# Kernel optimization log

Measured on AMD Instinct MI355X. Metric: run time of the kernel, lower is better.

Reference implementation:

```python
import jax, jax.numpy as jnp
import numpy as np

H = 32  # hidden_size
NUM_LAYERS = 3
INPUT_SIZE = 64
STD = 0.1


def setup_inputs() -> dict:
    key = jax.random.key(0)
    ks = jax.random.split(key, 2 * NUM_LAYERS + 2)
    inp = {}
    inp["x"] = jax.random.normal(ks[0], (256, 2048, INPUT_SIZE), dtype=jnp.float32)
    in_dim = INPUT_SIZE
    for l in range(NUM_LAYERS):
        inp[f"W_ih{l}"] = STD * jax.random.normal(ks[1 + 2 * l], (4 * H, in_dim), dtype=jnp.float32)
        inp[f"W_hh{l}"] = STD * jax.random.normal(ks[2 + 2 * l], (4 * H, H), dtype=jnp.float32)
        inp[f"b{l}"] = jnp.zeros((4 * H,), dtype=jnp.float32)  # b_ih + b_hh, both init to 0
        in_dim = H
    inp["W_out"] = STD * jax.random.normal(ks[-1], (1, H), dtype=jnp.float32)
    inp["b_out"] = jnp.zeros((1,), dtype=jnp.float32)
    return inp


def _lstm_layer(x, W_ih, W_hh, b):
    # x: [B, T, D_in] -> h_seq: [B, T, H]
    B = x.shape[0]
    # precompute input-to-gate projections for all timesteps (one big GEMM)
    xg = jnp.einsum('btd,gd->btg', x, W_ih) + b          # [B, T, 4H]
    xg = jnp.swapaxes(xg, 0, 1)                           # [T, B, 4H]
    W_hh_T = W_hh.T                                       # [H, 4H]

    def step(carry, xg_t):
        h, c = carry
        g = xg_t + h @ W_hh_T                             # [B, 4H]
        i = jax.nn.sigmoid(g[:, 0 * H:1 * H])
        f = jax.nn.sigmoid(g[:, 1 * H:2 * H])
        gg = jnp.tanh(g[:, 2 * H:3 * H])
        o = jax.nn.sigmoid(g[:, 3 * H:4 * H])
        c = f * c + i * gg
        h = o * jnp.tanh(c)
        return (h, c), h

    h0 = jnp.zeros((B, H), dtype=x.dtype)
    c0 = jnp.zeros((B, H), dtype=x.dtype)
    _, h_seq = jax.lax.scan(step, (h0, c0), xg)           # h_seq: [T, B, H]
    return jnp.swapaxes(h_seq, 0, 1)                      # [B, T, H]


def reference(x, W_ih0, W_hh0, b0, W_ih1, W_hh1, b1, W_ih2, W_hh2, b2, W_out, b_out):
    h = _lstm_layer(x, W_ih0, W_hh0, b0)
    h = _lstm_layer(h, W_ih1, W_hh1, b1)
    h = _lstm_layer(h, W_ih2, W_hh2, b2)
    last = h[:, -1, :]                                    # [B, H]
    return last @ W_out.T + b_out                         # [B, 1]
```

## Files before the change

kernel.cpp:

```cpp
#include <hip/hip_runtime.h>


typedef float v2f __attribute__((ext_vector_type(2)));

constexpr int T_SEQ  = 2048;
constexpr int HID    = 32;
constexpr int CH     = 16;
constexpr int NCHUNK = T_SEQ / CH;
constexpr int NPHASE = NCHUNK + 5;

__device__ __forceinline__ float sigmoid_f(float x) { return 1.0f / (1.0f + __expf(-x)); }
__device__ __forceinline__ float tanh_f(float x)    { return 1.0f - 2.0f / (__expf(2.0f * x) + 1.0f); }

#define GLOAD_LDS16(gsrc, ldst)                                                              \
    __builtin_amdgcn_global_load_lds((const __attribute__((address_space(1))) void*)(gsrc), \
                                     (__attribute__((address_space(3))) void*)(ldst),        \
                                     16, 0, 0)
#define KEEPV(x) asm volatile("" : "+v"(x))

template<int N4>
__device__ __forceinline__ void feed_chunk(int l, const float* in, int stride,
                                           v2f (*xg)[64],
                                           const v2f (&wA)[N4 * 2], const v2f (&wB)[N4 * 2],
                                           float bAv, float bBv)
{
#pragma unroll
    for (int tt = 0; tt < CH; ++tt) {
        const float4* xt = reinterpret_cast<const float4*>(in + tt * stride);
        v2f aA = {bAv, 0.f}, aB = {bBv, 0.f};
#pragma unroll
        for (int i = 0; i < N4; ++i) {
            const float4 v = xt[i];
            const v2f lo = {v.x, v.y}, hi = {v.z, v.w};
            aA = lo * wA[2*i] + aA;  aA = hi * wA[2*i+1] + aA;
            aB = lo * wB[2*i] + aB;  aB = hi * wB[2*i+1] + aB;
        }
        v2f o; o.x = aA.x + aA.y; o.y = aB.x + aB.y;
        xg[tt][l] = o;
    }
}

__device__ __forceinline__ void recur_chunk(int l, const v2f (*xg)[64],
                                            float* hbp, float (*hr)[HID],
                                            const v2f (&wA)[16], const v2f (&wB)[16],
                                            float& c, float& hreg)
{
#pragma unroll
    for (int tt = 0; tt < CH; ++tt) {
        const v2f xgv = xg[tt][l];
        asm volatile("s_waitcnt lgkmcnt(0)" ::: "memory");
        const float4* h4 = reinterpret_cast<const float4*>(hbp);
        v2f aA = {xgv.x, 0.f}, aB = {xgv.y, 0.f};
#pragma unroll
        for (int i = 0; i < 8; ++i) {
            const float4 v = h4[i];
            const v2f lo = {v.x, v.y}, hi = {v.z, v.w};
            aA = lo * wA[2*i] + aA;  aA = hi * wA[2*i+1] + aA;
            aB = lo * wB[2*i] + aB;  aB = hi * wB[2*i+1] + aB;
        }
        const float ga = aA.x + aA.y, gb = aB.x + aB.y;
        const float sA = sigmoid_f(ga);
        const float tb = tanh_f(l < 32 ? gb : 0.5f * gb);
        const float vB = (l < 32) ? tb : fmaf(0.5f, tb, 0.5f);
        const float fv = __shfl_xor(sA, 32);
        const float ov = __shfl_xor(vB, 32);
        const float cn = fmaf(fv, c, sA * vB);
        const float hn = ov * tanh_f(cn);
        if (l < HID) {
            c = cn; hreg = hn;
            hbp[l] = hn;
            if (hr) hr[tt][l] = hn;
        }
    }
}

__global__ __launch_bounds__(384, 2)
void lstm3_spec_kernel(const float* __restrict__ x,
                       const float* __restrict__ W_ih0, const float* __restrict__ W_hh0, const float* __restrict__ b0,
                       const float* __restrict__ W_ih1, const float* __restrict__ W_hh1, const float* __restrict__ b1,
                       const float* __restrict__ W_ih2, const float* __restrict__ W_hh2, const float* __restrict__ b2,
                       const float* __restrict__ W_out, const float* __restrict__ b_out,
                       float* __restrict__ out)
{
    const int bi = blockIdx.x;
    const int w  = threadIdx.x >> 6;
    const int l  = threadIdx.x & 63;

    __shared__ float xstage[CH * 64];
    __shared__ v2f   xg0[2][CH][64];
    __shared__ v2f   xg1[2][CH][64];
    __shared__ v2f   xg2[2][CH][64];
    __shared__ float h0r[2][CH][HID];
    __shared__ float h1r[2][CH][HID];
    __shared__ float hb[3][HID];

    if (w == 0) {
        __builtin_amdgcn_s_setprio(1);
        v2f wA[16], wB[16];
        const v2f* pA = reinterpret_cast<const v2f*>(W_hh0 + l * 32);
        const v2f* pB = reinterpret_cast<const v2f*>(W_hh0 + (l + 64) * 32);
#pragma unroll
        for (int i = 0; i < 16; ++i) { wA[i] = pA[i]; KEEPV(wA[i]); wB[i] = pB[i]; KEEPV(wB[i]); }
        if (l < HID) hb[0][l] = 0.f;
        float c = 0.f, hreg = 0.f;
        __syncthreads();
        for (int p = 0; p < NPHASE; ++p) {
            const int ci = p - 1;
            if (ci >= 0 && ci < NCHUNK)
                recur_chunk(l, xg0[ci & 1], hb[0], h0r[ci & 1], wA, wB, c, hreg);
            __syncthreads();
        }
    } else if (w == 1) {
        __builtin_amdgcn_s_setprio(1);
        v2f wA[16], wB[16];
        const v2f* pA = reinterpret_cast<const v2f*>(W_hh1 + l * 32);
        const v2f* pB = reinterpret_cast<const v2f*>(W_hh1 + (l + 64) * 32);
#pragma unroll
        for (int i = 0; i < 16; ++i) { wA[i] = pA[i]; KEEPV(wA[i]); wB[i] = pB[i]; KEEPV(wB[i]); }
        if (l < HID) hb[1][l] = 0.f;
        float c = 0.f, hreg = 0.f;
        __syncthreads();
        for (int p = 0; p < NPHASE; ++p) {
            const int ci = p - 3;
            if (ci >= 0 && ci < NCHUNK)
                recur_chunk(l, xg1[ci & 1], hb[1], h1r[ci & 1], wA, wB, c, hreg);
            __syncthreads();
        }
    } else if (w == 2) {
        __builtin_amdgcn_s_setprio(1);
        v2f wA[16], wB[16];
        const v2f* pA = reinterpret_cast<const v2f*>(W_hh2 + l * 32);
        const v2f* pB = reinterpret_cast<const v2f*>(W_hh2 + (l + 64) * 32);
#pragma unroll
        for (int i = 0; i < 16; ++i) { wA[i] = pA[i]; KEEPV(wA[i]); wB[i] = pB[i]; KEEPV(wB[i]); }
        const float woutv = (l < HID) ? W_out[l] : 0.f;
        if (l < HID) hb[2][l] = 0.f;
        float c = 0.f, hreg = 0.f;
        __syncthreads();
        for (int p = 0; p < NPHASE; ++p) {
            const int ci = p - 5;
            if (ci >= 0 && ci < NCHUNK)
                recur_chunk(l, xg2[ci & 1], hb[2], (float(*)[HID])nullptr, wA, wB, c, hreg);
            __syncthreads();
        }
        float s = (l < HID) ? hreg * woutv : 0.f;
#pragma unroll
        for (int off = 16; off; off >>= 1) s += __shfl_xor(s, off);
        if (l == 0) out[bi] = s + b_out[0];
    } else if (w == 3) {
        v2f wA[32], wB[32];
        const v2f* pA = reinterpret_cast<const v2f*>(W_ih0 + l * 64);
        const v2f* pB = reinterpret_cast<const v2f*>(W_ih0 + (l + 64) * 64);
#pragma unroll
        for (int i = 0; i < 32; ++i) { wA[i] = pA[i]; KEEPV(wA[i]); wB[i] = pB[i]; KEEPV(wB[i]); }
        const float bAv = b0[l], bBv = b0[l + 64];
        const float* src = x + (size_t)bi * T_SEQ * 64;
        __syncthreads();
        for (int p = 0; p < NPHASE; ++p) {
            if (p < NCHUNK) {
                const float* ns = src + (size_t)p * CH * 64;
#pragma unroll
                for (int i = 0; i < 4; ++i)
                    GLOAD_LDS16(ns + i * 256 + l * 4, &xstage[i * 256 + l * 4]);
                asm volatile("s_waitcnt vmcnt(0)" ::: "memory");
                feed_chunk<16>(l, xstage, 64, xg0[p & 1], wA, wB, bAv, bBv);
            }
            __syncthreads();
        }
    } else if (w == 4) {
        v2f wA[16], wB[16];
        const v2f* pA = reinterpret_cast<const v2f*>(W_ih1 + l * 32);
        const v2f* pB = reinterpret_cast<const v2f*>(W_ih1 + (l + 64) * 32);
#pragma unroll
        for (int i = 0; i < 16; ++i) { wA[i] = pA[i]; KEEPV(wA[i]); wB[i] = pB[i]; KEEPV(wB[i]); }
        const float bAv = b1[l], bBv = b1[l + 64];
        __syncthreads();
        for (int p = 0; p < NPHASE; ++p) {
            const int ci = p - 2;
            if (ci >= 0 && ci < NCHUNK)
                feed_chunk<8>(l, &h0r[ci & 1][0][0], HID, xg1[ci & 1], wA, wB, bAv, bBv);
            __syncthreads();
        }
    } else {
        v2f wA[16], wB[16];
        const v2f* pA = reinterpret_cast<const v2f*>(W_ih2 + l * 32);
        const v2f* pB = reinterpret_cast<const v2f*>(W_ih2 + (l + 64) * 32);
#pragma unroll
        for (int i = 0; i < 16; ++i) { wA[i] = pA[i]; KEEPV(wA[i]); wB[i] = pB[i]; KEEPV(wB[i]); }
        const float bAv = b2[l], bBv = b2[l + 64];
        __syncthreads();
        for (int p = 0; p < NPHASE; ++p) {
            const int ci = p - 4;
            if (ci >= 0 && ci < NCHUNK)
                feed_chunk<8>(l, &h1r[ci & 1][0][0], HID, xg2[ci & 1], wA, wB, bAv, bBv);
            __syncthreads();
        }
    }
}

extern "C" void kernel_launch(void* const* d_in, const int* in_sizes, int n_in,
                              void* d_out, int out_size, void* d_ws, size_t ws_size,
                              hipStream_t stream) {
    const float* x      = (const float*)d_in[0];
    const float* W_ih0  = (const float*)d_in[1];
    const float* W_hh0  = (const float*)d_in[2];
    const float* b0     = (const float*)d_in[3];
    const float* W_ih1  = (const float*)d_in[4];
    const float* W_hh1  = (const float*)d_in[5];
    const float* b1     = (const float*)d_in[6];
    const float* W_ih2  = (const float*)d_in[7];
    const float* W_hh2  = (const float*)d_in[8];
    const float* b2     = (const float*)d_in[9];
    const float* W_out  = (const float*)d_in[10];
    const float* b_out  = (const float*)d_in[11];

    lstm3_spec_kernel<<<256, 384, 0, stream>>>(x,
                                               W_ih0, W_hh0, b0,
                                               W_ih1, W_hh1, b1,
                                               W_ih2, W_hh2, b2,
                                               W_out, b_out,
                                               (float*)d_out);
}
```

Baseline: 699.8 us.

## Fuse next-layer input projection into recurrence waves and broadcast h via bpermute

Cuts the block from six waves to four. Each recurrent wave now computes the next layer's input projection right after its own step, which removes the separate feed waves and the h0r/h1r LDS round trip and shortens the pipeline by two phases. The hidden state is now broadcast to registers with ds_bpermute instead of being written to and read back from LDS. The layer-0 x loads are double-buffered so the global load overlaps the feed computation. The gate dot products are also split into two accumulators for more ILP. In exchange, each recurrent step carries more work on the serial critical path and uses more registers.

Result: slower. 1.022 ms (+46.0%).

```diff
diff --git a/kernel.cpp b/kernel.cpp
--- a/kernel.cpp
+++ b/kernel.cpp
@@ -7,7 +7,7 @@
 constexpr int HID    = 32;
 constexpr int CH     = 16;
 constexpr int NCHUNK = T_SEQ / CH;
-constexpr int NPHASE = NCHUNK + 5;
+constexpr int NPHASE = NCHUNK + 3;
 
 __device__ __forceinline__ float sigmoid_f(float x) { return 1.0f / (1.0f + __expf(-x)); }
 __device__ __forceinline__ float tanh_f(float x)    { return 1.0f - 2.0f / (__expf(2.0f * x) + 1.0f); }
@@ -18,47 +18,29 @@
                                      16, 0, 0)
 #define KEEPV(x) asm volatile("" : "+v"(x))
 
-template<int N4>
-__device__ __forceinline__ void feed_chunk(int l, const float* in, int stride,
-                                           v2f (*xg)[64],
-                                           const v2f (&wA)[N4 * 2], const v2f (&wB)[N4 * 2],
-                                           float bAv, float bBv)
+template<bool PROD>
+__device__ __forceinline__ void rec_chunk(int l, int a0v,
+    const v2f* __restrict__ xg_in, v2f* __restrict__ xg_out,
+    const v2f (&whA)[16], const v2f (&whB)[16],
+    const v2f* wiA, const v2f* wiB, float biA, float biB,
+    v2f (&hb2)[16], float& c, float& hreg)
 {
+    v2f xgr[CH];
+#pragma unroll
+    for (int tt = 0; tt < CH; ++tt) xgr[tt] = xg_in[tt * 64 + l];
+
 #pragma unroll
     for (int tt = 0; tt < CH; ++tt) {
-        const float4* xt = reinterpret_cast<const float4*>(in + tt * stride);
-        v2f aA = {bAv, 0.f}, aB = {bBv, 0.f};
-#pragma unroll
-        for (int i = 0; i < N4; ++i) {
-            const float4 v = xt[i];
-            const v2f lo = {v.x, v.y}, hi = {v.z, v.w};
-            aA = lo * wA[2*i] + aA;  aA = hi * wA[2*i+1] + aA;
-            aB = lo * wB[2*i] + aB;  aB = hi * wB[2*i+1] + aB;
-        }
-        v2f o; o.x = aA.x + aA.y; o.y = aB.x + aB.y;
-        xg[tt][l] = o;
-    }
-}
-
-__device__ __forceinline__ void recur_chunk(int l, const v2f (*xg)[64],
-                                            float* hbp, float (*hr)[HID],
-                                            const v2f (&wA)[16], const v2f (&wB)[16],
-                                            float& c, float& hreg)
-{
-#pragma unroll
-    for (int tt = 0; tt < CH; ++tt) {
-        const v2f xgv = xg[tt][l];
-        asm volatile("s_waitcnt lgkmcnt(0)" ::: "memory");
-        const float4* h4 = reinterpret_cast<const float4*>(hbp);
-        v2f aA = {xgv.x, 0.f}, aB = {xgv.y, 0.f};
-#pragma unroll
-        for (int i = 0; i < 8; ++i) {
-            const float4 v = h4[i];
-            const v2f lo = {v.x, v.y}, hi = {v.z, v.w};
-            aA = lo * wA[2*i] + aA;  aA = hi * wA[2*i+1] + aA;
-            aB = lo * wB[2*i] + aB;  aB = hi * wB[2*i+1] + aB;
-        }
-        const float ga = aA.x + aA.y, gb = aB.x + aB.y;
+        v2f aA0 = {xgr[tt].x, 0.f}, aA1 = {0.f, 0.f};
+        v2f aB0 = {xgr[tt].y, 0.f}, aB1 = {0.f, 0.f};
+#pragma unroll
+        for (int j = 0; j < 16; j += 2) {
+            aA0 = hb2[j]   * whA[j]   + aA0;  aB0 = hb2[j]   * whB[j]   + aB0;
+            aA1 = hb2[j+1] * whA[j+1] + aA1;  aB1 = hb2[j+1] * whB[j+1] + aB1;
+        }
+        const float ga = (aA0.x + aA1.x) + (aA0.y + aA1.y);
+        const float gb = (aB0.x + aB1.x) + (aB0.y + aB1.y);
+
         const float sA = sigmoid_f(ga);
         const float tb = tanh_f(l < 32 ? gb : 0.5f * gb);
         const float vB = (l < 32) ? tb : fmaf(0.5f, tb, 0.5f);
@@ -66,88 +48,138 @@
         const float ov = __shfl_xor(vB, 32);
         const float cn = fmaf(fv, c, sA * vB);
         const float hn = ov * tanh_f(cn);
-        if (l < HID) {
-            c = cn; hreg = hn;
-            hbp[l] = hn;
-            if (hr) hr[tt][l] = hn;
+        c = cn; hreg = hn;
+
+        const int hbits = __float_as_int(hn);
+#pragma unroll
+        for (int j = 0; j < 16; ++j) {
+            const float bx = __int_as_float(__builtin_amdgcn_ds_bpermute(a0v + 8*j,     hbits));
+            const float by = __int_as_float(__builtin_amdgcn_ds_bpermute(a0v + 8*j + 4, hbits));
+            hb2[j] = (v2f){bx, by};
+        }
+
+        if constexpr (PROD) {
+            v2f pA = {biA, 0.f}, pB = {biB, 0.f};
+#pragma unroll
+            for (int j = 0; j < 16; ++j) { pA = hb2[j] * wiA[j] + pA; pB = hb2[j] * wiB[j] + pB; }
+            xg_out[tt * 64 + l] = (v2f){pA.x + pA.y, pB.x + pB.y};
         }
     }
 }
 
-__global__ __launch_bounds__(384, 2)
-void lstm3_spec_kernel(const float* __restrict__ x,
-                       const float* __restrict__ W_ih0, const float* __restrict__ W_hh0, const float* __restrict__ b0,
-                       const float* __restrict__ W_ih1, const float* __restrict__ W_hh1, const float* __restrict__ b1,
-                       const float* __restrict__ W_ih2, const float* __restrict__ W_hh2, const float* __restrict__ b2,
-                       const float* __restrict__ W_out, const float* __restrict__ b_out,
-                       float* __restrict__ out)
+__device__ __forceinline__ void feed0_chunk(int l, const float* __restrict__ xs,
+    v2f* __restrict__ xg_out,
+    const v2f (&wA)[32], const v2f (&wB)[32], float bAv, float bBv)
+{
+#pragma unroll
+    for (int tt = 0; tt < CH; ++tt) {
+        const float4* xt = reinterpret_cast<const float4*>(xs + tt * 64);
+        v2f aA0 = {bAv, 0.f}, aA1 = {0.f, 0.f}, aB0 = {bBv, 0.f}, aB1 = {0.f, 0.f};
+#pragma unroll
+        for (int i = 0; i < 16; ++i) {
+            const float4 v = xt[i];
+            const v2f lo = {v.x, v.y}, hi = {v.z, v.w};
+            aA0 = lo * wA[2*i] + aA0;  aA1 = hi * wA[2*i+1] + aA1;
+            aB0 = lo * wB[2*i] + aB0;  aB1 = hi * wB[2*i+1] + aB1;
+        }
+        xg_out[tt * 64 + l] = (v2f){(aA0.x + aA1.x) + (aA0.y + aA1.y),
+                                    (aB0.x + aB1.x) + (aB0.y + aB1.y)};
+    }
+}
+
+__global__ __launch_bounds__(256, 1)
+void lstm3_fused_kernel(const float* __restrict__ x,
+    const float* __restrict__ W_ih0, const float* __restrict__ W_hh0, const float* __restrict__ b0,
+    const float* __restrict__ W_ih1, const float* __restrict__ W_hh1, const float* __restrict__ b1,
+    const float* __restrict__ W_ih2, const float* __restrict__ W_hh2, const float* __restrict__ b2,
+    const float* __restrict__ W_out, const float* __restrict__ b_out,
+    float* __restrict__ out)
 {
     const int bi = blockIdx.x;
     const int w  = threadIdx.x >> 6;
     const int l  = threadIdx.x & 63;
 
-    __shared__ float xstage[CH * 64];
     __shared__ v2f   xg0[2][CH][64];
     __shared__ v2f   xg1[2][CH][64];
     __shared__ v2f   xg2[2][CH][64];
-    __shared__ float h0r[2][CH][HID];
-    __shared__ float h1r[2][CH][HID];
-    __shared__ float hb[3][HID];
+    __shared__ float xstage[2][CH * 64];
+
+    int a0v = 0; asm volatile("" : "+v"(a0v));
 
     if (w == 0) {
-        __builtin_amdgcn_s_setprio(1);
-        v2f wA[16], wB[16];
-        const v2f* pA = reinterpret_cast<const v2f*>(W_hh0 + l * 32);
-        const v2f* pB = reinterpret_cast<const v2f*>(W_hh0 + (l + 64) * 32);
-#pragma unroll
-        for (int i = 0; i < 16; ++i) { wA[i] = pA[i]; KEEPV(wA[i]); wB[i] = pB[i]; KEEPV(wB[i]); }
-        if (l < HID) hb[0][l] = 0.f;
+        v2f whA[16], whB[16], wiA[16], wiB[16];
+        const v2f* hA = reinterpret_cast<const v2f*>(W_hh0 + l * 32);
+        const v2f* hB = reinterpret_cast<const v2f*>(W_hh0 + (l + 64) * 32);
+        const v2f* iA = reinterpret_cast<const v2f*>(W_ih1 + l * 32);
+        const v2f* iB = reinterpret_cast<const v2f*>(W_ih1 + (l + 64) * 32);
+#pragma unroll
+        for (int i = 0; i < 16; ++i) {
+            whA[i] = hA[i]; KEEPV(whA[i]); whB[i] = hB[i]; KEEPV(whB[i]);
+            wiA[i] = iA[i]; KEEPV(wiA[i]); wiB[i] = iB[i]; KEEPV(wiB[i]);
+        }
+        const float biA = b1[l], biB = b1[l + 64];
+        v2f hb2[16];
+#pragma unroll
+        for (int i = 0; i < 16; ++i) hb2[i] = (v2f){0.f, 0.f};
         float c = 0.f, hreg = 0.f;
         __syncthreads();
         for (int p = 0; p < NPHASE; ++p) {
             const int ci = p - 1;
             if (ci >= 0 && ci < NCHUNK)
-                recur_chunk(l, xg0[ci & 1], hb[0], h0r[ci & 1], wA, wB, c, hreg);
+                rec_chunk<true>(l, a0v, &xg0[ci & 1][0][0], &xg1[ci & 1][0][0],
+                                whA, whB, wiA, wiB, biA, biB, hb2, c, hreg);
             __syncthreads();
         }
     } else if (w == 1) {
-        __builtin_amdgcn_s_setprio(1);
-        v2f wA[16], wB[16];
-        const v2f* pA = reinterpret_cast<const v2f*>(W_hh1 + l * 32);
-        const v2f* pB = reinterpret_cast<const v2f*>(W_hh1 + (l + 64) * 32);
-#pragma unroll
-        for (int i = 0; i < 16; ++i) { wA[i] = pA[i]; KEEPV(wA[i]); wB[i] = pB[i]; KEEPV(wB[i]); }
-        if (l < HID) hb[1][l] = 0.f;
+        v2f whA[16], whB[16], wiA[16], wiB[16];
+        const v2f* hA = reinterpret_cast<const v2f*>(W_hh1 + l * 32);
+        const v2f* hB = reinterpret_cast<const v2f*>(W_hh1 + (l + 64) * 32);
+        const v2f* iA = reinterpret_cast<const v2f*>(W_ih2 + l * 32);
+        const v2f* iB = reinterpret_cast<const v2f*>(W_ih2 + (l + 64) * 32);
+#pragma unroll
+        for (int i = 0; i < 16; ++i) {
+            whA[i] = hA[i]; KEEPV(whA[i]); whB[i] = hB[i]; KEEPV(whB[i]);
+            wiA[i] = iA[i]; KEEPV(wiA[i]); wiB[i] = iB[i]; KEEPV(wiB[i]);
+        }
+        const float biA = b2[l], biB = b2[l + 64];
+        v2f hb2[16];
+#pragma unroll
+        for (int i = 0; i < 16; ++i) hb2[i] = (v2f){0.f, 0.f};
+        float c = 0.f, hreg = 0.f;
+        __syncthreads();
+        for (int p = 0; p < NPHASE; ++p) {
+            const int ci = p - 2;
+            if (ci >= 0 && ci < NCHUNK)
+                rec_chunk<true>(l, a0v, &xg1[ci & 1][0][0], &xg2[ci & 1][0][0],
+                                whA, whB, wiA, wiB, biA, biB, hb2, c, hreg);
+            __syncthreads();
+        }
+    } else if (w == 2) {
+        v2f whA[16], whB[16];
+        const v2f* hA = reinterpret_cast<const v2f*>(W_hh2 + l * 32);
+        const v2f* hB = reinterpret_cast<const v2f*>(W_hh2 + (l + 64) * 32);
+#pragma unroll
+        for (int i = 0; i < 16; ++i) {
+            whA[i] = hA[i]; KEEPV(whA[i]); whB[i] = hB[i]; KEEPV(whB[i]);
+        }
+        const float woutv = W_out[l & 31];
+        v2f hb2[16];
+#pragma unroll
+        for (int i = 0; i < 16; ++i) hb2[i] = (v2f){0.f, 0.f};
         float c = 0.f, hreg = 0.f;
         __syncthreads();
         for (int p = 0; p < NPHASE; ++p) {
             const int ci = p - 3;
             if (ci >= 0 && ci < NCHUNK)
-                recur_chunk(l, xg1[ci & 1], hb[1], h1r[ci & 1], wA, wB, c, hreg);
-            __syncthreads();
-        }
-    } else if (w == 2) {
-        __builtin_amdgcn_s_setprio(1);
-        v2f wA[16], wB[16];
-        const v2f* pA = reinterpret_cast<const v2f*>(W_hh2 + l * 32);
-        const v2f* pB = reinterpret_cast<const v2f*>(W_hh2 + (l + 64) * 32);
-#pragma unroll
-        for (int i = 0; i < 16; ++i) { wA[i] = pA[i]; KEEPV(wA[i]); wB[i] = pB[i]; KEEPV(wB[i]); }
-        const float woutv = (l < HID) ? W_out[l] : 0.f;
-        if (l < HID) hb[2][l] = 0.f;
-        float c = 0.f, hreg = 0.f;
-        __syncthreads();
-        for (int p = 0; p < NPHASE; ++p) {
-            const int ci = p - 5;
-            if (ci >= 0 && ci < NCHUNK)
-                recur_chunk(l, xg2[ci & 1], hb[2], (float(*)[HID])nullptr, wA, wB, c, hreg);
+                rec_chunk<false>(l, a0v, &xg2[ci & 1][0][0], nullptr,
+                                 whA, whB, nullptr, nullptr, 0.f, 0.f, hb2, c, hreg);
             __syncthreads();
         }
         float s = (l < HID) ? hreg * woutv : 0.f;
 #pragma unroll
-        for (int off = 16; off; off >>= 1) s += __shfl_xor(s, off);
+        for (int off = 32; off; off >>= 1) s += __shfl_xor(s, off);
         if (l == 0) out[bi] = s + b_out[0];
-    } else if (w == 3) {
+    } else {
         v2f wA[32], wB[32];
         const v2f* pA = reinterpret_cast<const v2f*>(W_ih0 + l * 64);
         const v2f* pB = reinterpret_cast<const v2f*>(W_ih0 + (l + 64) * 64);
@@ -155,44 +187,20 @@
         for (int i = 0; i < 32; ++i) { wA[i] = pA[i]; KEEPV(wA[i]); wB[i] = pB[i]; KEEPV(wB[i]); }
         const float bAv = b0[l], bBv = b0[l + 64];
         const float* src = x + (size_t)bi * T_SEQ * 64;
-        __syncthreads();
-        for (int p = 0; p < NPHASE; ++p) {
-            if (p < NCHUNK) {
-                const float* ns = src + (size_t)p * CH * 64;
+#pragma unroll
+        for (int i = 0; i < 4; ++i)
+            GLOAD_LDS16(src + i * 256 + l * 4, &xstage[0][i * 256 + l * 4]);
+        __syncthreads();
+        for (int p = 0; p < NPHASE; ++p) {
+            if (p + 1 < NCHUNK) {
+                const float* ns = src + (size_t)(p + 1) * CH * 64;
+                float* dst = &xstage[(p + 1) & 1][0];
 #pragma unroll
                 for (int i = 0; i < 4; ++i)
-                    GLOAD_LDS16(ns + i * 256 + l * 4, &xstage[i * 256 + l * 4]);
-                asm volatile("s_waitcnt vmcnt(0)" ::: "memory");
-                feed_chunk<16>(l, xstage, 64, xg0[p & 1], wA, wB, bAv, bBv);
+                    GLOAD_LDS16(ns + i * 256 + l * 4, dst + i * 256 + l * 4);
             }
-            __syncthreads();
-        }
-    } else if (w == 4) {
-        v2f wA[16], wB[16];
-        const v2f* pA = reinterpret_cast<const v2f*>(W_ih1 + l * 32);
-        const v2f* pB = reinterpret_cast<const v2f*>(W_ih1 + (l + 64) * 32);
-#pragma unroll
-        for (int i = 0; i < 16; ++i) { wA[i] = pA[i]; KEEPV(wA[i]); wB[i] = pB[i]; KEEPV(wB[i]); }
-        const float bAv = b1[l], bBv = b1[l + 64];
-        __syncthreads();
-        for (int p = 0; p < NPHASE; ++p) {
-            const int ci = p - 2;
-            if (ci >= 0 && ci < NCHUNK)
-                feed_chunk<8>(l, &h0r[ci & 1][0][0], HID, xg1[ci & 1], wA, wB, bAv, bBv);
-            __syncthreads();
-        }
-    } else {
-        v2f wA[16], wB[16];
-        const v2f* pA = reinterpret_cast<const v2f*>(W_ih2 + l * 32);
-        const v2f* pB = reinterpret_cast<const v2f*>(W_ih2 + (l + 64) * 32);
-#pragma unroll
-        for (int i = 0; i < 16; ++i) { wA[i] = pA[i]; KEEPV(wA[i]); wB[i] = pB[i]; KEEPV(wB[i]); }
-        const float bAv = b2[l], bBv = b2[l + 64];
-        __syncthreads();
-        for (int p = 0; p < NPHASE; ++p) {
-            const int ci = p - 4;
-            if (ci >= 0 && ci < NCHUNK)
-                feed_chunk<8>(l, &h1r[ci & 1][0][0], HID, xg2[ci & 1], wA, wB, bAv, bBv);
+            if (p < NCHUNK)
+                feed0_chunk(l, xstage[p & 1], &xg0[p & 1][0][0], wA, wB, bAv, bBv);
             __syncthreads();
         }
     }
@@ -214,10 +222,10 @@
     const float* W_out  = (const float*)d_in[10];
     const float* b_out  = (const float*)d_in[11];
 
-    lstm3_spec_kernel<<<256, 384, 0, stream>>>(x,
-                                               W_ih0, W_hh0, b0,
-                                               W_ih1, W_hh1, b1,
-                                               W_ih2, W_hh2, b2,
-                                               W_out, b_out,
-                                               (float*)d_out);
-}
+    lstm3_fused_kernel<<<256, 256, 0, stream>>>(x,
+                                                W_ih0, W_hh0, b0,
+                                                W_ih1, W_hh1, b1,
+                                                W_ih2, W_hh2, b2,
+                                                W_out, b_out,
+                                                (float*)d_out);
+}
```

## Broadcast recurrent hidden state via readlane instead of LDS, prefetch x double-buffered

Applied to the files above, without the earlier changes.

The recurrent waves now broadcast the new hidden state to every lane with 32 readlane instructions into SGPR-backed registers. This replaces writing it to LDS and reading it back behind an lgkmcnt wait, taking the LDS round trip off the serial critical path of each timestep. Gate math uses hardware rcp and per-lane constants instead of selects. The input-projection wave double-buffers the x staging area so the next chunk's global load overlaps the current chunk's compute. The readlane chain adds scalar-path serialization and register pressure, and all lanes now compute c/h redundantly.

Result: slower. 757.6 us (+8.3%).

```diff
diff --git a/kernel.cpp b/kernel.cpp
--- a/kernel.cpp
+++ b/kernel.cpp
@@ -4,13 +4,9 @@
 typedef float v2f __attribute__((ext_vector_type(2)));
 
 constexpr int T_SEQ  = 2048;
-constexpr int HID    = 32;
 constexpr int CH     = 16;
 constexpr int NCHUNK = T_SEQ / CH;
 constexpr int NPHASE = NCHUNK + 5;
-
-__device__ __forceinline__ float sigmoid_f(float x) { return 1.0f / (1.0f + __expf(-x)); }
-__device__ __forceinline__ float tanh_f(float x)    { return 1.0f - 2.0f / (__expf(2.0f * x) + 1.0f); }
 
 #define GLOAD_LDS16(gsrc, ldst)                                                              \
     __builtin_amdgcn_global_load_lds((const __attribute__((address_space(1))) void*)(gsrc), \
@@ -18,132 +14,183 @@
                                      16, 0, 0)
 #define KEEPV(x) asm volatile("" : "+v"(x))
 
-template<int N4>
-__device__ __forceinline__ void feed_chunk(int l, const float* in, int stride,
-                                           v2f (*xg)[64],
-                                           const v2f (&wA)[N4 * 2], const v2f (&wB)[N4 * 2],
-                                           float bAv, float bBv)
-{
+__device__ __forceinline__ float rcp_f(float x) { return __builtin_amdgcn_rcpf(x); }
+
+template<bool RING>
+__device__ __forceinline__ void rec_chunk_rl(int l,
+    const v2f* __restrict__ xg_in,
+    float* __restrict__ ring_out,
+    const float (&whA)[32], const float (&whB)[32],
+    float (&hs)[32], float& c, float& hreg,
+    float mt, float ca, float cb)
+{
+    v2f xgr[CH];
+#pragma unroll
+    for (int tt = 0; tt < CH; ++tt) xgr[tt] = xg_in[tt * 64 + l];
+
 #pragma unroll
     for (int tt = 0; tt < CH; ++tt) {
-        const float4* xt = reinterpret_cast<const float4*>(in + tt * stride);
-        v2f aA = {bAv, 0.f}, aB = {bBv, 0.f};
-#pragma unroll
-        for (int i = 0; i < N4; ++i) {
-            const float4 v = xt[i];
-            const v2f lo = {v.x, v.y}, hi = {v.z, v.w};
-            aA = lo * wA[2*i] + aA;  aA = hi * wA[2*i+1] + aA;
-            aB = lo * wB[2*i] + aB;  aB = hi * wB[2*i+1] + aB;
-        }
-        v2f o; o.x = aA.x + aA.y; o.y = aB.x + aB.y;
-        xg[tt][l] = o;
-    }
-}
-
-__device__ __forceinline__ void recur_chunk(int l, const v2f (*xg)[64],
-                                            float* hbp, float (*hr)[HID],
-                                            const v2f (&wA)[16], const v2f (&wB)[16],
-                                            float& c, float& hreg)
+        float aA0 = xgr[tt].x, aA1 = 0.f, aB0 = xgr[tt].y, aB1 = 0.f;
+#pragma unroll
+        for (int k = 0; k < 32; k += 2) {
+            aA0 = fmaf(hs[k],     whA[k],     aA0);
+            aB0 = fmaf(hs[k],     whB[k],     aB0);
+            aA1 = fmaf(hs[k + 1], whA[k + 1], aA1);
+            aB1 = fmaf(hs[k + 1], whB[k + 1], aB1);
+        }
+        const float ga = aA0 + aA1, gb = aB0 + aB1;
+
+        const float sA = rcp_f(1.0f + __expf(-ga));
+        const float eb = __expf(mt * gb);
+        const float tb = fmaf(-2.0f, rcp_f(eb + 1.0f), 1.0f);
+        const float vB = fmaf(ca, tb, cb);
+
+        const float fv = __shfl_xor(sA, 32);
+        const float ov = __shfl_xor(vB, 32);
+        const float cn = fmaf(fv, c, sA * vB);
+        const float ec = __expf(2.0f * cn);
+        const float hn = ov * fmaf(-2.0f, rcp_f(ec + 1.0f), 1.0f);
+        c = cn; hreg = hn;
+
+        if constexpr (RING) { if (l < 32) ring_out[tt * 32 + l] = hn; }
+
+        const int hbits = __float_as_int(hn);
+#pragma unroll
+        for (int k = 0; k < 32; ++k)
+            hs[k] = __int_as_float(__builtin_amdgcn_readlane(hbits, k));
+    }
+}
+
+__device__ __forceinline__ void feed_h_chunk(int l, const float* __restrict__ hr,
+    v2f* __restrict__ xg_out, const v2f (&wA)[16], const v2f (&wB)[16],
+    float bA, float bB)
 {
 #pragma unroll
     for (int tt = 0; tt < CH; ++tt) {
-        const v2f xgv = xg[tt][l];
-        asm volatile("s_waitcnt lgkmcnt(0)" ::: "memory");
-        const float4* h4 = reinterpret_cast<const float4*>(hbp);
-        v2f aA = {xgv.x, 0.f}, aB = {xgv.y, 0.f};
+        const float4* h4 = reinterpret_cast<const float4*>(hr + tt * 32);
+        v2f a0 = {bA, 0.f}, a1 = {0.f, 0.f}, b0 = {bB, 0.f}, b1 = {0.f, 0.f};
 #pragma unroll
         for (int i = 0; i < 8; ++i) {
             const float4 v = h4[i];
             const v2f lo = {v.x, v.y}, hi = {v.z, v.w};
-            aA = lo * wA[2*i] + aA;  aA = hi * wA[2*i+1] + aA;
-            aB = lo * wB[2*i] + aB;  aB = hi * wB[2*i+1] + aB;
-        }
-        const float ga = aA.x + aA.y, gb = aB.x + aB.y;
-        const float sA = sigmoid_f(ga);
-        const float tb = tanh_f(l < 32 ? gb : 0.5f * gb);
-        const float vB = (l < 32) ? tb : fmaf(0.5f, tb, 0.5f);
-        const float fv = __shfl_xor(sA, 32);
-        const float ov = __shfl_xor(vB, 32);
-        const float cn = fmaf(fv, c, sA * vB);
-        const float hn = ov * tanh_f(cn);
-        if (l < HID) {
-            c = cn; hreg = hn;
-            hbp[l] = hn;
-            if (hr) hr[tt][l] = hn;
-        }
+            a0 = lo * wA[2*i] + a0;  a1 = hi * wA[2*i+1] + a1;
+            b0 = lo * wB[2*i] + b0;  b1 = hi * wB[2*i+1] + b1;
+        }
+        xg_out[tt * 64 + l] = (v2f){(a0.x + a1.x) + (a0.y + a1.y),
+                                    (b0.x + b1.x) + (b0.y + b1.y)};
+    }
+}
+
+__device__ __forceinline__ void feed0_chunk(int l, const float* __restrict__ xs,
+    v2f* __restrict__ xg_out, const v2f (&wA)[32], const v2f (&wB)[32],
+    float bA, float bB)
+{
+#pragma unroll
+    for (int tt = 0; tt < CH; ++tt) {
+        const float4* xt = reinterpret_cast<const float4*>(xs + tt * 64);
+        v2f a0 = {bA, 0.f}, a1 = {0.f, 0.f}, b0 = {bB, 0.f}, b1 = {0.f, 0.f};
+#pragma unroll
+        for (int i = 0; i < 16; ++i) {
+            const float4 v = xt[i];
+            const v2f lo = {v.x, v.y}, hi = {v.z, v.w};
+            a0 = lo * wA[2*i] + a0;  a1 = hi * wA[2*i+1] + a1;
+            b0 = lo * wB[2*i] + b0;  b1 = hi * wB[2*i+1] + b1;
+        }
+        xg_out[tt * 64 + l] = (v2f){(a0.x + a1.x) + (a0.y + a1.y),
+                                    (b0.x + b1.x) + (b0.y + b1.y)};
     }
 }
 
 __global__ __launch_bounds__(384, 2)
-void lstm3_spec_kernel(const float* __restrict__ x,
-                       const float* __restrict__ W_ih0, const float* __restrict__ W_hh0, const float* __restrict__ b0,
-                       const float* __restrict__ W_ih1, const float* __restrict__ W_hh1, const float* __restrict__ b1,
-                       const float* __restrict__ W_ih2, const float* __restrict__ W_hh2, const float* __restrict__ b2,
-                       const float* __restrict__ W_out, const float* __restrict__ b_out,
-                       float* __restrict__ out)
+void lstm3_rl_kernel(const float* __restrict__ x,
+    const float* __restrict__ W_ih0, const float* __restrict__ W_hh0, const float* __restrict__ b0,
+    const float* __restrict__ W_ih1, const float* __restrict__ W_hh1, const float* __restrict__ b1,
+    const float* __restrict__ W_ih2, const float* __restrict__ W_hh2, const float* __restrict__ b2,
+    const float* __restrict__ W_out, const float* __restrict__ b_out,
+    float* __restrict__ out)
 {
     const int bi = blockIdx.x;
     const int w  = threadIdx.x >> 6;
     const int l  = threadIdx.x & 63;
 
-    __shared__ float xstage[CH * 64];
     __shared__ v2f   xg0[2][CH][64];
     __shared__ v2f   xg1[2][CH][64];
     __shared__ v2f   xg2[2][CH][64];
-    __shared__ float h0r[2][CH][HID];
-    __shared__ float h1r[2][CH][HID];
-    __shared__ float hb[3][HID];
+    __shared__ float h0r[2][CH][32];
+    __shared__ float h1r[2][CH][32];
+    __shared__ float xstage[2][CH * 64];
 
     if (w == 0) {
         __builtin_amdgcn_s_setprio(1);
-        v2f wA[16], wB[16];
-        const v2f* pA = reinterpret_cast<const v2f*>(W_hh0 + l * 32);
-        const v2f* pB = reinterpret_cast<const v2f*>(W_hh0 + (l + 64) * 32);
-#pragma unroll
-        for (int i = 0; i < 16; ++i) { wA[i] = pA[i]; KEEPV(wA[i]); wB[i] = pB[i]; KEEPV(wB[i]); }
-        if (l < HID) hb[0][l] = 0.f;
+        float whA[32], whB[32];
+#pragma unroll
+        for (int k = 0; k < 32; ++k) {
+            whA[k] = W_hh0[l * 32 + k];        KEEPV(whA[k]);
+            whB[k] = W_hh0[(l + 64) * 32 + k]; KEEPV(whB[k]);
+        }
+        const float mt = (l < 32) ? 2.f : 1.f;
+        const float ca = (l < 32) ? 1.f : 0.5f;
+        const float cb = (l < 32) ? 0.f : 0.5f;
+        float hs[32];
+#pragma unroll
+        for (int k = 0; k < 32; ++k) hs[k] = 0.f;
         float c = 0.f, hreg = 0.f;
         __syncthreads();
         for (int p = 0; p < NPHASE; ++p) {
             const int ci = p - 1;
             if (ci >= 0 && ci < NCHUNK)
-                recur_chunk(l, xg0[ci & 1], hb[0], h0r[ci & 1], wA, wB, c, hreg);
+                rec_chunk_rl<true>(l, &xg0[ci & 1][0][0], &h0r[ci & 1][0][0],
+                                   whA, whB, hs, c, hreg, mt, ca, cb);
             __syncthreads();
         }
     } else if (w == 1) {
         __builtin_amdgcn_s_setprio(1);
-        v2f wA[16], wB[16];
-        const v2f* pA = reinterpret_cast<const v2f*>(W_hh1 + l * 32);
-        const v2f* pB = reinterpret_cast<const v2f*>(W_hh1 + (l + 64) * 32);
-#pragma unroll
-        for (int i = 0; i < 16; ++i) { wA[i] = pA[i]; KEEPV(wA[i]); wB[i] = pB[i]; KEEPV(wB[i]); }
-        if (l < HID) hb[1][l] = 0.f;
+        float whA[32], whB[32];
+#pragma unroll
+        for (int k = 0; k < 32; ++k) {
+            whA[k] = W_hh1[l * 32 + k];        KEEPV(whA[k]);
+            whB[k] = W_hh1[(l + 64) * 32 + k]; KEEPV(whB[k]);
+        }
+        const float mt = (l < 32) ? 2.f : 1.f;
+        const float ca = (l < 32) ? 1.f : 0.5f;
+        const float cb = (l < 32) ? 0.f : 0.5f;
+        float hs[32];
+#pragma unroll
+        for (int k = 0; k < 32; ++k) hs[k] = 0.f;
         float c = 0.f, hreg = 0.f;
         __syncthreads();
         for (int p = 0; p < NPHASE; ++p) {
             const int ci = p - 3;
             if (ci >= 0 && ci < NCHUNK)
-                recur_chunk(l, xg1[ci & 1], hb[1], h1r[ci & 1], wA, wB, c, hreg);
+                rec_chunk_rl<true>(l, &xg1[ci & 1][0][0], &h1r[ci & 1][0][0],
+                                   whA, whB, hs, c, hreg, mt, ca, cb);
             __syncthreads();
         }
     } else if (w == 2) {
         __builtin_amdgcn_s_setprio(1);
-        v2f wA[16], wB[16];
-        const v2f* pA = reinterpret_cast<const v2f*>(W_hh2 + l * 32);
-        const v2f* pB = reinterpret_cast<const v2f*>(W_hh2 + (l + 64) * 32);
-#pragma unroll
-        for (int i = 0; i < 16; ++i) { wA[i] = pA[i]; KEEPV(wA[i]); wB[i] = pB[i]; KEEPV(wB[i]); }
-        const float woutv = (l < HID) ? W_out[l] : 0.f;
-        if (l < HID) hb[2][l] = 0.f;
+        float whA[32], whB[32];
+#pragma unroll
+        for (int k = 0; k < 32; ++k) {
+            whA[k] = W_hh2[l * 32 + k];        KEEPV(whA[k]);
+            whB[k] = W_hh2[(l + 64) * 32 + k]; KEEPV(whB[k]);
+        }
+        const float mt = (l < 32) ? 2.f : 1.f;
+        const float ca = (l < 32) ? 1.f : 0.5f;
+        const float cb = (l < 32) ? 0.f : 0.5f;
+        const float woutv = W_out[l & 31];
+        float hs[32];
+#pragma unroll
+        for (int k = 0; k < 32; ++k) hs[k] = 0.f;
         float c = 0.f, hreg = 0.f;
         __syncthreads();
         for (int p = 0; p < NPHASE; ++p) {
             const int ci = p - 5;
             if (ci >= 0 && ci < NCHUNK)
-                recur_chunk(l, xg2[ci & 1], hb[2], (float(*)[HID])nullptr, wA, wB, c, hreg);
-            __syncthreads();
-        }
-        float s = (l < HID) ? hreg * woutv : 0.f;
+                rec_chunk_rl<false>(l, &xg2[ci & 1][0][0], nullptr,
+                                    whA, whB, hs, c, hreg, mt, ca, cb);
+            __syncthreads();
+        }
+        float s = (l < 32) ? hreg * woutv : 0.f;
 #pragma unroll
         for (int off = 16; off; off >>= 1) s += __shfl_xor(s, off);
         if (l == 0) out[bi] = s + b_out[0];
@@ -155,16 +202,20 @@
         for (int i = 0; i < 32; ++i) { wA[i] = pA[i]; KEEPV(wA[i]); wB[i] = pB[i]; KEEPV(wB[i]); }
         const float bAv = b0[l], bBv = b0[l + 64];
         const float* src = x + (size_t)bi * T_SEQ * 64;
-        __syncthreads();
-        for (int p = 0; p < NPHASE; ++p) {
-            if (p < NCHUNK) {
-                const float* ns = src + (size_t)p * CH * 64;
+#pragma unroll
+        for (int i = 0; i < 4; ++i)
+            GLOAD_LDS16(src + i * 256 + l * 4, &xstage[0][i * 256 + l * 4]);
+        __syncthreads();
+        for (int p = 0; p < NPHASE; ++p) {
+            if (p + 1 < NCHUNK) {
+                const float* ns = src + (size_t)(p + 1) * CH * 64;
+                float* dst = &xstage[(p + 1) & 1][0];
 #pragma unroll
                 for (int i = 0; i < 4; ++i)
-                    GLOAD_LDS16(ns + i * 256 + l * 4, &xstage[i * 256 + l * 4]);
-                asm volatile("s_waitcnt vmcnt(0)" ::: "memory");
-                feed_chunk<16>(l, xstage, 64, xg0[p & 1], wA, wB, bAv, bBv);
+                    GLOAD_LDS16(ns + i * 256 + l * 4, dst + i * 256 + l * 4);
             }
+            if (p < NCHUNK)
+                feed0_chunk(l, xstage[p & 1], &xg0[p & 1][0][0], wA, wB, bAv, bBv);
             __syncthreads();
         }
     } else if (w == 4) {
@@ -178,7 +229,7 @@
         for (int p = 0; p < NPHASE; ++p) {
             const int ci = p - 2;
             if (ci >= 0 && ci < NCHUNK)
-                feed_chunk<8>(l, &h0r[ci & 1][0][0], HID, xg1[ci & 1], wA, wB, bAv, bBv);
+                feed_h_chunk(l, &h0r[ci & 1][0][0], &xg1[ci & 1][0][0], wA, wB, bAv, bBv);
             __syncthreads();
         }
     } else {
@@ -192,7 +243,7 @@
         for (int p = 0; p < NPHASE; ++p) {
             const int ci = p - 4;
             if (ci >= 0 && ci < NCHUNK)
-                feed_chunk<8>(l, &h1r[ci & 1][0][0], HID, xg2[ci & 1], wA, wB, bAv, bBv);
+                feed_h_chunk(l, &h1r[ci & 1][0][0], &xg2[ci & 1][0][0], wA, wB, bAv, bBv);
             __syncthreads();
         }
     }
@@ -214,10 +265,10 @@
     const float* W_out  = (const float*)d_in[10];
     const float* b_out  = (const float*)d_in[11];
 
-    lstm3_spec_kernel<<<256, 384, 0, stream>>>(x,
-                                               W_ih0, W_hh0, b0,
-                                               W_ih1, W_hh1, b1,
-                                               W_ih2, W_hh2, b2,
-                                               W_out, b_out,
-                                               (float*)d_out);
-}
+    lstm3_rl_kernel<<<256, 384, 0, stream>>>(x,
+                                             W_ih0, W_hh0, b0,
+                                             W_ih1, W_hh1, b1,
+                                             W_ih2, W_hh2, b2,
+                                             W_out, b_out,
+                                             (float*)d_out);
+}
```
